# Kernel tuning notes

Hardware: AMD Instinct MI355X
Metric: run time of the kernel (lower is better)

Reference implementation:

```python
import jax, jax.numpy as jnp
import numpy as np

# --- constants (UnscaleSST / SST range assumed; see notes) ---
SST_MEAN = 13.5
SST_STD = 8.0
SST_MIN = -2.0
SST_MAX = 35.0
WIN = 11          # pytorch-msssim default gaussian window size
SIGMA = 1.5       # default gaussian sigma
K1, K2 = 0.01, 0.03
DATA_RANGE = 1.0


def _gauss_win():
    coords = np.arange(WIN, dtype=np.float64) - WIN // 2
    g = np.exp(-(coords ** 2) / (2.0 * SIGMA ** 2))
    g = g / g.sum()
    return jnp.asarray(g, dtype=jnp.float32)


def _blur(x, g):
    # separable valid-padding gaussian filter, NCHW single channel
    dn = ('NCHW', 'OIHW', 'NCHW')
    kh = g.reshape(1, 1, WIN, 1)
    kw = g.reshape(1, 1, 1, WIN)
    x = jax.lax.conv_general_dilated(x, kh, (1, 1), 'VALID', dimension_numbers=dn)
    x = jax.lax.conv_general_dilated(x, kw, (1, 1), 'VALID', dimension_numbers=dn)
    return x


def _unnormalize(x):
    x = x * SST_STD + SST_MEAN               # UnscaleSST (inverse standardization)
    x = (x - SST_MIN) / (SST_MAX - SST_MIN)  # min-max to [0, 1]
    return jnp.nan_to_num(x)


def _ssim(X, Y):
    g = _gauss_win()
    C1 = (K1 * DATA_RANGE) ** 2
    C2 = (K2 * DATA_RANGE) ** 2
    mu1 = _blur(X, g)
    mu2 = _blur(Y, g)
    mu1_sq, mu2_sq, mu12 = mu1 * mu1, mu2 * mu2, mu1 * mu2
    sigma1_sq = _blur(X * X, g) - mu1_sq
    sigma2_sq = _blur(Y * Y, g) - mu2_sq
    sigma12 = _blur(X * Y, g) - mu12
    cs_map = (2.0 * sigma12 + C2) / (sigma1_sq + sigma2_sq + C2)
    ssim_map = ((2.0 * mu12 + C1) / (mu1_sq + mu2_sq + C1)) * cs_map
    # per-channel mean over spatial dims -> [B, C]
    ssim_pc = ssim_map.mean(axis=(2, 3))
    ssim_pc = jax.nn.relu(ssim_pc)  # nonnegative_ssim=True
    return ssim_pc.mean()           # size_average=True


def setup_inputs() -> dict:
    key = jax.random.key(0)
    k1, k2 = jax.random.split(key)
    shape = (64, 1, 512, 512)
    pred = jax.random.normal(k1, shape, dtype=jnp.float32)
    target = jax.random.normal(k2, shape, dtype=jnp.float32)
    return {"pred": pred, "target": target}


def reference(pred, target):
    return _ssim(_unnormalize(pred), _unnormalize(target))
```

## Files before the change

kernel.cpp:

```cpp
#include <hip/hip_runtime.h>
#include <math.h>


typedef float v2f __attribute__((ext_vector_type(2)));

#define WIN 11
#define IMG 512
#define OUTW 502
#define BAND 32
#define RY 4
#define COLS2 516

constexpr float A_SC  = 8.0f / 37.0f;
constexpr float TWO_B = 2.0f * (15.5f / 37.0f);
constexpr float TWO_C1 = 2.0f * 1e-4f;
constexpr float TWO_C2 = 2.0f * 9e-4f;

__global__ __launch_bounds__(512, 4)
void ssim_main(const float* __restrict__ X, const float* __restrict__ Y,
               float* __restrict__ ws)
{
    __shared__ __align__(16) v2f sP[2][RY][COLS2];
    __shared__ float sW[WIN];
    __shared__ float sRed[8];

    const int tid  = threadIdx.x;
    const int band = blockIdx.x;
    const int b    = blockIdx.y;
    const int y0   = band * BAND;

    if (tid == 0) {
        double g[WIN]; double sum = 0.0;
        for (int k = 0; k < WIN; ++k) { double c = k - 5; g[k] = exp(-(c * c) / 4.5); sum += g[k]; }
        for (int k = 0; k < WIN; ++k) sW[k] = (float)(g[k] / sum);
    }
    __syncthreads();
    float w[WIN];
    #pragma unroll
    for (int k = 0; k < WIN; ++k)
        w[k] = __uint_as_float(__builtin_amdgcn_readfirstlane(__float_as_uint(sW[k])));

    const float* __restrict__ Xb = X + (size_t)b * (IMG * (size_t)IMG);
    const float* __restrict__ Yb = Y + (size_t)b * (IMG * (size_t)IMG);

    const int x  = tid;
    const int r  = tid >> 7;
    const int gi = (tid >> 6) & 1;
    const int s  = tid & 63;
    const int x0 = 4 * (s + 64 * gi);

    float acc = 0.0f;

    v2f psd[10];
    #pragma unroll
    for (int i = 0; i < 10; ++i) {
        const uint32_t idx = (uint32_t)(y0 + i) * IMG + (uint32_t)x;
        const float xv = Xb[idx], yv = Yb[idx];
        v2f t; t.x = fmaf(xv + yv, A_SC, TWO_B); t.y = (xv - yv) * A_SC;
        psd[i] = t;
    }

    #pragma unroll 1
    for (int c = 0; c < BAND / RY; ++c) {
        const int ybase = y0 + c * RY;
        if (ybase < OUTW) {
            v2f vsd[RY], vq[RY];
            #pragma unroll
            for (int rr = 0; rr < RY; ++rr) { vsd[rr] = (v2f)0.0f; vq[rr] = (v2f)0.0f; }

            #pragma unroll
            for (int j = 0; j < 10; ++j) {
                const v2f a = psd[j];
                const v2f q = a * a;
                #pragma unroll
                for (int rr = 0; rr < RY; ++rr) {
                    const int k = j - rr;
                    if (k >= 0 && k < WIN) {
                        const float wk = w[k];
                        vsd[rr] += wk * a;
                        vq[rr]  += wk * q;
                    }
                }
            }
            v2f nw[RY];
            #pragma unroll
            for (int jj = 0; jj < RY; ++jj) {
                const int j = 10 + jj;
                int yi = ybase + j; yi = yi < IMG - 1 ? yi : IMG - 1;
                const uint32_t idx = (uint32_t)yi * IMG + (uint32_t)x;
                const float xv = Xb[idx], yv = Yb[idx];
                v2f a; a.x = fmaf(xv + yv, A_SC, TWO_B); a.y = (xv - yv) * A_SC;
                const v2f q = a * a;
                #pragma unroll
                for (int rr = 0; rr < RY; ++rr) {
                    const int k = j - rr;
                    if (k >= 0 && k < WIN) {
                        const float wk = w[k];
                        vsd[rr] += wk * a;
                        vq[rr]  += wk * q;
                    }
                }
                nw[jj] = a;
            }
            #pragma unroll
            for (int i = 0; i < 10 - RY; ++i) psd[i] = psd[i + RY];
            #pragma unroll
            for (int i = 0; i < RY; ++i) psd[10 - RY + i] = nw[i];

            __syncthreads();
            #pragma unroll
            for (int rr = 0; rr < RY; ++rr) {
                sP[0][rr][x] = vsd[rr];
                sP[1][rr][x] = vq[rr];
            }
            __syncthreads();

            const int yo = ybase + r;
            if (yo < OUTW && x0 < OUTW) {
                v2f Hsd[4], Hq[4];
                #pragma unroll
                for (int p = 0; p < 2; ++p) {
                    v2f a0 = (v2f)0.0f, a1 = (v2f)0.0f, a2 = (v2f)0.0f, a3 = (v2f)0.0f;
                    const float4* q4 = (const float4*)&sP[p][r][x0];
                    #pragma unroll
                    for (int j4 = 0; j4 < 7; ++j4) {
                        const float4 qq = q4[j4];
                        #pragma unroll
                        for (int h = 0; h < 2; ++h) {
                            const int j = 2 * j4 + h;
                            v2f col; col.x = h ? qq.z : qq.x; col.y = h ? qq.w : qq.y;
                            if (j - 0 >= 0 && j - 0 < WIN) a0 += w[j]     * col;
                            if (j - 1 >= 0 && j - 1 < WIN) a1 += w[j - 1] * col;
                            if (j - 2 >= 0 && j - 2 < WIN) a2 += w[j - 2] * col;
                            if (j - 3 >= 0 && j - 3 < WIN) a3 += w[j - 3] * col;
                        }
                    }
                    if (p == 0) { Hsd[0] = a0; Hsd[1] = a1; Hsd[2] = a2; Hsd[3] = a3; }
                    else        { Hq[0]  = a0; Hq[1]  = a1; Hq[2]  = a2; Hq[3]  = a3; }
                }
                #pragma unroll
                for (int i = 0; i < 4; ++i) {
                    if (x0 + i < OUTW) {
                        const v2f m2 = Hsd[i] * Hsd[i];
                        const v2f sg = Hq[i] - m2;
                        const float na = m2.x - m2.y + TWO_C1;
                        const float da = m2.x + m2.y + TWO_C1;
                        const float nb = sg.x - sg.y + TWO_C2;
                        const float db = sg.x + sg.y + TWO_C2;
                        acc = fmaf(na * nb, __builtin_amdgcn_rcpf(da * db), acc);
                    }
                }
            }
        }
    }

    #pragma unroll
    for (int off = 32; off > 0; off >>= 1) acc += __shfl_down(acc, off, 64);
    if ((tid & 63) == 0) sRed[tid >> 6] = acc;
    __syncthreads();
    if (tid == 0) {
        float t = 0.f;
        #pragma unroll
        for (int i = 0; i < 8; ++i) t += sRed[i];
        atomicAdd(&ws[b], t);
    }
}

__global__ void ssim_finalize(const float* __restrict__ ws, float* __restrict__ out)
{
    const int t = threadIdx.x;
    float v = ws[t] * (1.0f / (502.0f * 502.0f));
    v = v > 0.f ? v : 0.f;
    #pragma unroll
    for (int off = 32; off > 0; off >>= 1) v += __shfl_down(v, off, 64);
    if (t == 0) out[0] = v * (1.0f / 64.0f);
}

extern "C" void kernel_launch(void* const* d_in, const int* in_sizes, int n_in,
                              void* d_out, int out_size, void* d_ws, size_t ws_size,
                              hipStream_t stream)
{
    const float* pred   = (const float*)d_in[0];
    const float* target = (const float*)d_in[1];
    float* out = (float*)d_out;
    float* ws  = (float*)d_ws;

    hipMemsetAsync(ws, 0, 64 * sizeof(float), stream);
    ssim_main<<<dim3(16, 64), 512, 0, stream>>>(pred, target, ws);
    ssim_finalize<<<1, 64, 0, stream>>>(ws, out);
}
```

Baseline: 165.1 us.

## Double-buffer vertical/horizontal pass stages and double the row band height

Restructures the band loop into a software pipeline. Each iteration issues the next chunk's global loads first, then runs the horizontal pass on the previous chunk from one shared buffer while the vertical pass writes the other. This halves the barriers per chunk and hides load latency behind horizontal compute. Band height doubles to 64, which halves the grid to 512 blocks and reduces redundant halo row loads, at the cost of fewer blocks for occupancy and twice the shared memory per block.

```diff
diff --git a/kernel.cpp b/kernel.cpp
--- a/kernel.cpp
+++ b/kernel.cpp
@@ -7,8 +7,9 @@
 #define WIN 11
 #define IMG 512
 #define OUTW 502
-#define BAND 32
+#define BAND 64
 #define RY 4
+#define NCHUNK (BAND / RY)
 #define COLS2 516
 
 constexpr float A_SC  = 8.0f / 37.0f;
@@ -20,7 +21,7 @@
 void ssim_main(const float* __restrict__ X, const float* __restrict__ Y,
                float* __restrict__ ws)
 {
-    __shared__ __align__(16) v2f sP[2][RY][COLS2];
+    __shared__ __align__(16) v2f sP[2][2][RY][COLS2];
     __shared__ float sW[WIN];
     __shared__ float sRed[8];
 
@@ -61,67 +62,31 @@
     }
 
     #pragma unroll 1
-    for (int c = 0; c < BAND / RY; ++c) {
-        const int ybase = y0 + c * RY;
-        if (ybase < OUTW) {
-            v2f vsd[RY], vq[RY];
-            #pragma unroll
-            for (int rr = 0; rr < RY; ++rr) { vsd[rr] = (v2f)0.0f; vq[rr] = (v2f)0.0f; }
-
-            #pragma unroll
-            for (int j = 0; j < 10; ++j) {
-                const v2f a = psd[j];
-                const v2f q = a * a;
-                #pragma unroll
-                for (int rr = 0; rr < RY; ++rr) {
-                    const int k = j - rr;
-                    if (k >= 0 && k < WIN) {
-                        const float wk = w[k];
-                        vsd[rr] += wk * a;
-                        vq[rr]  += wk * q;
-                    }
-                }
-            }
-            v2f nw[RY];
+    for (int c = -1; c < NCHUNK; ++c) {
+        const int vchunk = c + 1;
+        const bool dovert = (vchunk < NCHUNK);
+        const int nbase = y0 + vchunk * RY;
+
+        float fx[RY], fy[RY];
+        if (dovert) {
             #pragma unroll
             for (int jj = 0; jj < RY; ++jj) {
-                const int j = 10 + jj;
-                int yi = ybase + j; yi = yi < IMG - 1 ? yi : IMG - 1;
+                int yi = nbase + 10 + jj; yi = yi < IMG - 1 ? yi : IMG - 1;
                 const uint32_t idx = (uint32_t)yi * IMG + (uint32_t)x;
-                const float xv = Xb[idx], yv = Yb[idx];
-                v2f a; a.x = fmaf(xv + yv, A_SC, TWO_B); a.y = (xv - yv) * A_SC;
-                const v2f q = a * a;
-                #pragma unroll
-                for (int rr = 0; rr < RY; ++rr) {
-                    const int k = j - rr;
-                    if (k >= 0 && k < WIN) {
-                        const float wk = w[k];
-                        vsd[rr] += wk * a;
-                        vq[rr]  += wk * q;
-                    }
-                }
-                nw[jj] = a;
-            }
-            #pragma unroll
-            for (int i = 0; i < 10 - RY; ++i) psd[i] = psd[i + RY];
-            #pragma unroll
-            for (int i = 0; i < RY; ++i) psd[10 - RY + i] = nw[i];
-
-            __syncthreads();
-            #pragma unroll
-            for (int rr = 0; rr < RY; ++rr) {
-                sP[0][rr][x] = vsd[rr];
-                sP[1][rr][x] = vq[rr];
-            }
-            __syncthreads();
-
+                fx[jj] = Xb[idx]; fy[jj] = Yb[idx];
+            }
+        }
+
+        if (c >= 0) {
+            const int ybase = y0 + c * RY;
             const int yo = ybase + r;
             if (yo < OUTW && x0 < OUTW) {
+                const int bufc = c & 1;
                 v2f Hsd[4], Hq[4];
                 #pragma unroll
                 for (int p = 0; p < 2; ++p) {
                     v2f a0 = (v2f)0.0f, a1 = (v2f)0.0f, a2 = (v2f)0.0f, a3 = (v2f)0.0f;
-                    const float4* q4 = (const float4*)&sP[p][r][x0];
+                    const float4* q4 = (const float4*)&sP[bufc][p][r][x0];
                     #pragma unroll
                     for (int j4 = 0; j4 < 7; ++j4) {
                         const float4 qq = q4[j4];
@@ -152,6 +117,57 @@
                 }
             }
         }
+
+        if (dovert) {
+            const int bufn = vchunk & 1;
+            v2f vsd[RY], vq[RY];
+            #pragma unroll
+            for (int rr = 0; rr < RY; ++rr) { vsd[rr] = (v2f)0.0f; vq[rr] = (v2f)0.0f; }
+
+            #pragma unroll
+            for (int j = 0; j < 10; ++j) {
+                const v2f a = psd[j];
+                const v2f q = a * a;
+                #pragma unroll
+                for (int rr = 0; rr < RY; ++rr) {
+                    const int k = j - rr;
+                    if (k >= 0 && k < WIN) {
+                        const float wk = w[k];
+                        vsd[rr] += wk * a;
+                        vq[rr]  += wk * q;
+                    }
+                }
+            }
+            v2f nw[RY];
+            #pragma unroll
+            for (int jj = 0; jj < RY; ++jj) {
+                const int j = 10 + jj;
+                v2f a; a.x = fmaf(fx[jj] + fy[jj], A_SC, TWO_B); a.y = (fx[jj] - fy[jj]) * A_SC;
+                const v2f q = a * a;
+                #pragma unroll
+                for (int rr = 0; rr < RY; ++rr) {
+                    const int k = j - rr;
+                    if (k >= 0 && k < WIN) {
+                        const float wk = w[k];
+                        vsd[rr] += wk * a;
+                        vq[rr]  += wk * q;
+                    }
+                }
+                nw[jj] = a;
+            }
+            #pragma unroll
+            for (int i = 0; i < 10 - RY; ++i) psd[i] = psd[i + RY];
+            #pragma unroll
+            for (int i = 0; i < RY; ++i) psd[10 - RY + i] = nw[i];
+
+            #pragma unroll
+            for (int rr = 0; rr < RY; ++rr) {
+                sP[bufn][0][rr][x] = vsd[rr];
+                sP[bufn][1][rr][x] = vq[rr];
+            }
+        }
+
+        __syncthreads();
     }
 
     #pragma unroll
@@ -186,6 +202,6 @@
     float* ws  = (float*)d_ws;
 
     hipMemsetAsync(ws, 0, 64 * sizeof(float), stream);
-    ssim_main<<<dim3(16, 64), 512, 0, stream>>>(pred, target, ws);
+    ssim_main<<<dim3(8, 64), 512, 0, stream>>>(pred, target, ws);
     ssim_finalize<<<1, 64, 0, stream>>>(ws, out);
 }
```

Result: faster. 159.2 us (-3.6%).
